# Optimization experiments

Hardware: AMD Instinct MI355X
Metric: run time of the kernel (lower is better)

## Reference

```python
import jax, jax.numpy as jnp
import numpy as np
from jax.scipy.linalg import expm

DIM = 64
TIMESTEPS = 1000
BATCH = 1024


def setup_inputs() -> dict:
    key = jax.random.key(0)
    k1, k2 = jax.random.split(key)
    inputs = jax.random.normal(k1, (BATCH, TIMESTEPS, DIM), dtype=jnp.float32)
    # Kernel: skew-symmetric (oscillatory) + small decay so expm(kernel*t) stays
    # bounded for t up to TIMESTEPS-1 (a random dense kernel would overflow).
    a = jax.random.normal(k2, (DIM, DIM), dtype=jnp.float32)
    kernel = 0.01 * (a - a.T) - 0.002 * jnp.eye(DIM, dtype=jnp.float32)
    return {"inputs": inputs, "kernel": kernel}


def reference(inputs, kernel):
    # matrix_exponentials[t] = expm(kernel * t), t = 0..T-1  -> [T, dim, dim]
    ts = jnp.arange(TIMESTEPS, dtype=kernel.dtype)
    mexp = jax.vmap(expm)(kernel[None, :, :] * ts[:, None, None])
    # trajs = einsum('tij,bj->bti'): propagate initial state inputs[:, 0, :]
    x0 = inputs[:, 0, :]  # [B, dim]
    return jnp.einsum('tij,bj->bti', mexp, x0)  # [B, T, dim]
```

## Files before the change

### kernel.cpp

```cpp
#include <hip/hip_runtime.h>

#define NMAT 1000
#define SA_PAD 68
#define LDM 72

#define SEEDF_OFF 2048000
#define X0B_OFF   8355840

typedef short short8 __attribute__((ext_vector_type(8)));
typedef float floatx4 __attribute__((ext_vector_type(4)));
typedef unsigned short ushortx4 __attribute__((ext_vector_type(4)));

__device__ __forceinline__ unsigned short f2bf(float f) {
    unsigned int u = __float_as_uint(f);
    u += 0x7fffu + ((u >> 16) & 1u);
    return (unsigned short)(u >> 16);
}

__device__ __forceinline__ void mm_core(const float* __restrict__ sA,
                                        const float* __restrict__ sB,
                                        int r0, int c0, float acc[4][4])
{
#pragma unroll
    for (int k = 0; k < 64; k += 4) {
        float4 b0 = *(const float4*)&sB[(k + 0) * SA_PAD + c0];
        float4 b1 = *(const float4*)&sB[(k + 1) * SA_PAD + c0];
        float4 b2 = *(const float4*)&sB[(k + 2) * SA_PAD + c0];
        float4 b3 = *(const float4*)&sB[(k + 3) * SA_PAD + c0];
#pragma unroll
        for (int u = 0; u < 4; ++u) {
            float4 a = *(const float4*)&sA[(r0 + u) * SA_PAD + k];
            acc[u][0] += a.x * b0.x + a.y * b1.x + a.z * b2.x + a.w * b3.x;
            acc[u][1] += a.x * b0.y + a.y * b1.y + a.z * b2.y + a.w * b3.y;
            acc[u][2] += a.x * b0.z + a.y * b1.z + a.z * b2.z + a.w * b3.z;
            acc[u][3] += a.x * b0.w + a.y * b1.w + a.z * b2.w + a.w * b3.w;
        }
    }
}

__device__ __forceinline__ void stageLDS(float* __restrict__ s, const float* __restrict__ g, int tid)
{
#pragma unroll
    for (int q = 0; q < 4; ++q) {
        int i4 = tid + 256 * q;
        int r = i4 >> 4, c4 = (i4 & 15) * 4;
        *(float4*)&s[r * SA_PAD + c4] = *(const float4*)&g[i4 * 4];
    }
}

__global__ __launch_bounds__(256) void k_build(const float* __restrict__ K,
                                               const float* __restrict__ in,
                                               float* __restrict__ ws)
{
    const int tid = threadIdx.x;
    unsigned short* tab16 = (unsigned short*)ws;
    unsigned short* x0b = (unsigned short*)((char*)ws + X0B_OFF);

    if (blockIdx.x != 0) {
        const int rb = (blockIdx.x - 1) * 64;
#pragma unroll
        for (int q = 0; q < 4; ++q) {
            int i4 = tid + 256 * q;
            int b = rb + (i4 >> 4), c4 = (i4 & 15) * 4;
            float4 v = *(const float4*)&in[(size_t)b * 64000 + c4];
            ushortx4 h = { f2bf(v.x), f2bf(v.y), f2bf(v.z), f2bf(v.w) };
            *(ushortx4*)&x0b[(size_t)b * 64 + c4] = h;
        }
        return;
    }

    __shared__ __align__(16) float smem[6 * 64 * SA_PAD];

#pragma unroll
    for (int q = 0; q < 4; ++q) {
        int i4 = tid + 256 * q;
        int r = i4 >> 4, c4 = (i4 & 15) * 4;
        *(float4*)&smem[r * SA_PAD + c4] = *(const float4*)&K[i4 * 4];
        ushortx4 id = {0, 0, 0, 0};
        if (r >= c4 && r < c4 + 4) ((unsigned short*)&id)[r - c4] = 0x3F80;
        *(ushortx4*)&tab16[r * 64 + c4] = id;
    }

    const float c1_ = 1.f, c2_ = 0.5f, c3_ = 1.f / 6.f, c4_ = 1.f / 24.f, c5_ = 1.f / 120.f,
                c6_ = 1.f / 720.f, c7_ = 1.f / 5040.f, c8_ = 1.f / 40320.f, c9_ = 1.f / 362880.f,
                c10_ = 1.f / 3628800.f, c11_ = 1.f / 39916800.f, c12_ = 1.f / 479001600.f;

    const signed char SD[14]  = {1, 2, 3, 5, 4, 5, 0, 1, 2, 3, 4, 5, 0, 1};
    const signed char SAi[14] = {0, 1, 1, 4, 5, 4, 5, 0, 1, 2, 3, 4, 5, 0};
    const signed char SBi[14] = {0, 0, 1, 3, 3, 4, 5, 0, 1, 2, 3, 4, 5, 0};
    const signed char SE[14]  = {-1, -1, -1, 0, 1, -1, -1, -1, -1, -1, -1, -1, -1, -1};
    const short       STt[14] = {-1, -1, -1, -1, 1, 2, 4, 8, 16, 32, 64, 128, 256, 512};

    const int r0 = (tid >> 4) * 4, c0 = (tid & 15) * 4;

#pragma unroll 1
    for (int st = 0; st < 14; ++st) {
        if (st == 3) {
            __syncthreads();
#pragma unroll
            for (int s = 0; s < 16; ++s) {
                int idx = tid + 256 * s;
                int r = idx >> 6, c = idx & 63;
                smem[4 * (64 * SA_PAD) + r * SA_PAD + c] =
                      c12_ * smem[3 * (64 * SA_PAD) + r * SA_PAD + c] + (r == c ? c8_ : 0.f)
                    + c9_  * smem[0 * (64 * SA_PAD) + r * SA_PAD + c]
                    + c10_ * smem[1 * (64 * SA_PAD) + r * SA_PAD + c]
                    + c11_ * smem[2 * (64 * SA_PAD) + r * SA_PAD + c];
            }
        }
        __syncthreads();
        const float* A = smem + (int)SAi[st] * (64 * SA_PAD);
        const float* B = smem + (int)SBi[st] * (64 * SA_PAD);
        float acc[4][4] = {};
        mm_core(A, B, r0, c0, acc);

        float cI = 0.f, cK = 0.f, cT2 = 0.f, cT3 = 0.f;
        const int epi = SE[st];
        if (epi == 0) { cI = c4_; cK = c5_; cT2 = c6_; cT3 = c7_; }
        if (epi == 1) { cI = 1.f; cK = c1_; cT2 = c2_; cT3 = c3_; }

        float* D = smem + (int)SD[st] * (64 * SA_PAD);
        float* sf = (STt[st] >= 0) ? (ws + SEEDF_OFF + (size_t)(st - 4) * 4096) : nullptr;
        unsigned short* tb = (STt[st] >= 0) ? (tab16 + (size_t)STt[st] * 4096) : nullptr;
#pragma unroll
        for (int u = 0; u < 4; ++u) {
            int r = r0 + u;
            float o[4];
#pragma unroll
            for (int v = 0; v < 4; ++v) {
                int c = c0 + v;
                float val = acc[u][v];
                if (epi >= 0) {
                    val += (r == c ? cI : 0.f)
                         + cK  * smem[0 * (64 * SA_PAD) + r * SA_PAD + c]
                         + cT2 * smem[1 * (64 * SA_PAD) + r * SA_PAD + c]
                         + cT3 * smem[2 * (64 * SA_PAD) + r * SA_PAD + c];
                }
                o[v] = val;
            }
            float4 vv = {o[0], o[1], o[2], o[3]};
            *(float4*)&D[r * SA_PAD + c0] = vv;
            if (sf) {
                *(float4*)&sf[r * 64 + c0] = vv;
                ushortx4 h = { f2bf(o[0]), f2bf(o[1]), f2bf(o[2]), f2bf(o[3]) };
                *(ushortx4*)&tb[r * 64 + c0] = h;
            }
        }
    }
}

__global__ __launch_bounds__(256) void k_pows(float* __restrict__ ws)
{
    __shared__ __align__(16) float s0[64 * SA_PAD], s1[64 * SA_PAD], s2[64 * SA_PAD];
    const int t = blockIdx.x;
    if (__popc(t) < 2) return;
    const float* seedF = ws + SEEDF_OFF;
    unsigned short* tab16 = (unsigned short*)ws;
    const int tid = threadIdx.x;
    const int r0 = (tid >> 4) * 4, c0 = (tid & 15) * 4;

    float* P = s0;
    float* Bs = s1;
    float* Cs = s2;

    int hb = 31 - __clz(t);
    stageLDS(P, seedF + (size_t)hb * 4096, tid);
    int rem = t & ~(1 << hb);

    float4 rg[4];
    {
        int b = 31 - __clz(rem);
        rem &= ~(1 << b);
        const float* g = seedF + (size_t)b * 4096;
#pragma unroll
        for (int q = 0; q < 4; ++q) rg[q] = *(const float4*)&g[(tid + 256 * q) * 4];
    }

    while (true) {
        __syncthreads();
#pragma unroll
        for (int q = 0; q < 4; ++q) {
            int i4 = tid + 256 * q;
            int rr = i4 >> 4, c4 = (i4 & 15) * 4;
            *(float4*)&Bs[rr * SA_PAD + c4] = rg[q];
        }
        int nb = -1;
        if (rem) {
            nb = 31 - __clz(rem);
            rem &= ~(1 << nb);
            const float* g = seedF + (size_t)nb * 4096;
#pragma unroll
            for (int q = 0; q < 4; ++q) rg[q] = *(const float4*)&g[(tid + 256 * q) * 4];
        }
        __syncthreads();
        float acc[4][4] = {};
        mm_core(P, Bs, r0, c0, acc);

        if (nb < 0) {
            unsigned short* C = tab16 + (size_t)t * 4096;
#pragma unroll
            for (int u = 0; u < 4; ++u) {
                ushortx4 h = { f2bf(acc[u][0]), f2bf(acc[u][1]),
                               f2bf(acc[u][2]), f2bf(acc[u][3]) };
                *(ushortx4*)&C[(r0 + u) * 64 + c0] = h;
            }
            return;
        }
#pragma unroll
        for (int u = 0; u < 4; ++u) {
            float4 vv = {acc[u][0], acc[u][1], acc[u][2], acc[u][3]};
            *(float4*)&Cs[(r0 + u) * SA_PAD + c0] = vv;
        }
        float* tmp = P; P = Cs; Cs = tmp;
    }
}

__global__ __launch_bounds__(256) void k_out(const float* __restrict__ ws,
                                             float* __restrict__ out)
{
    __shared__ __align__(16) unsigned short lM[64 * LDM];
    __shared__ __align__(16) unsigned short lX[128 * LDM];

    const unsigned short* tab16 = (const unsigned short*)ws;
    const unsigned short* x0b = (const unsigned short*)((const char*)ws + X0B_OFF);

    const int bx = blockIdx.x;
    const int t = bx >> 3;
    const int b0 = (bx & 7) * 128;
    const unsigned short* Mt = tab16 + (size_t)t * 4096;
    const int tid = threadIdx.x;

#pragma unroll
    for (int q = 0; q < 2; ++q) {
        int i8 = tid + 256 * q;
        int i = i8 >> 3, j8 = (i8 & 7) * 8;
        *(short8*)&lM[i * LDM + j8] = *(const short8*)&Mt[i8 * 8];
    }
#pragma unroll
    for (int q = 0; q < 4; ++q) {
        int i8 = tid + 256 * q;
        int bb = i8 >> 3, j8 = (i8 & 7) * 8;
        *(short8*)&lX[bb * LDM + j8] = *(const short8*)&x0b[(size_t)(b0 + bb) * 64 + j8];
    }
    __syncthreads();

    const int lane = tid & 63;
    const int w = tid >> 6;
    const int m = lane & 15;
    const int kg = lane >> 4;

#pragma unroll
    for (int mt = 0; mt < 2; ++mt) {
        const int mtile = w * 2 + mt;
        short8 a0 = *(const short8*)&lX[(mtile * 16 + m) * LDM + kg * 8];
        short8 a1 = *(const short8*)&lX[(mtile * 16 + m) * LDM + 32 + kg * 8];
#pragma unroll
        for (int n = 0; n < 4; ++n) {
            short8 bf0 = *(const short8*)&lM[(n * 16 + m) * LDM + kg * 8];
            short8 bf1 = *(const short8*)&lM[(n * 16 + m) * LDM + 32 + kg * 8];
            floatx4 acc = {0.f, 0.f, 0.f, 0.f};
            acc = __builtin_amdgcn_mfma_f32_16x16x32_bf16(a0, bf0, acc, 0, 0, 0);
            acc = __builtin_amdgcn_mfma_f32_16x16x32_bf16(a1, bf1, acc, 0, 0, 0);
            size_t base = (size_t)(b0 + mtile * 16 + kg * 4) * 64000 + (size_t)t * 64 + n * 16 + m;
            out[base + 0 * 64000] = acc[0];
            out[base + 1 * 64000] = acc[1];
            out[base + 2 * 64000] = acc[2];
            out[base + 3 * 64000] = acc[3];
        }
    }
}

extern "C" void kernel_launch(void* const* d_in, const int* in_sizes, int n_in,
                              void* d_out, int out_size, void* d_ws, size_t ws_size,
                              hipStream_t stream)
{
    const float* inp = (const float*)d_in[0];
    const float* K   = (const float*)d_in[1];
    float* out = (float*)d_out;
    float* ws  = (float*)d_ws;

    hipLaunchKernelGGL(k_build, dim3(17), dim3(256), 0, stream, K, inp, ws);
    hipLaunchKernelGGL(k_pows, dim3(NMAT), dim3(256), 0, stream, ws);
    hipLaunchKernelGGL(k_out, dim3(8000), dim3(256), 0, stream, ws, out);
}
```

Measured before the change: 590.8 us.

## Swap MFMA operands in output kernel for vectorized stores and drop LDS staging

The output kernel now passes the matrix as the A operand and x0 as the B operand, so each lane holds four consecutive output columns and can write one 16-byte vector store instead of four scattered scalar stores. The LDS staging and barrier are gone: operands load straight from global memory into registers, x0 is loaded once per thread, and each block loops over 8 timesteps with a 64-row batch tile. This targets the write-bandwidth-bound output of about 262 MB by coalescing stores along the contiguous dim axis, at the cost of repeated global reads of matrix tiles, which are expected to hit in cache.

```diff
diff --git a/kernel.cpp b/kernel.cpp
--- a/kernel.cpp
+++ b/kernel.cpp
@@ -2,7 +2,6 @@
 
 #define NMAT 1000
 #define SA_PAD 68
-#define LDM 72
 
 #define SEEDF_OFF 2048000
 #define X0B_OFF   8355840
@@ -218,54 +217,41 @@
 __global__ __launch_bounds__(256) void k_out(const float* __restrict__ ws,
                                              float* __restrict__ out)
 {
-    __shared__ __align__(16) unsigned short lM[64 * LDM];
-    __shared__ __align__(16) unsigned short lX[128 * LDM];
-
     const unsigned short* tab16 = (const unsigned short*)ws;
     const unsigned short* x0b = (const unsigned short*)((const char*)ws + X0B_OFF);
 
     const int bx = blockIdx.x;
-    const int t = bx >> 3;
-    const int b0 = (bx & 7) * 128;
-    const unsigned short* Mt = tab16 + (size_t)t * 4096;
+    const int tg = bx >> 4;
+    const int bt = bx & 15;
     const int tid = threadIdx.x;
-
-#pragma unroll
-    for (int q = 0; q < 2; ++q) {
-        int i8 = tid + 256 * q;
-        int i = i8 >> 3, j8 = (i8 & 7) * 8;
-        *(short8*)&lM[i * LDM + j8] = *(const short8*)&Mt[i8 * 8];
-    }
-#pragma unroll
-    for (int q = 0; q < 4; ++q) {
-        int i8 = tid + 256 * q;
-        int bb = i8 >> 3, j8 = (i8 & 7) * 8;
-        *(short8*)&lX[bb * LDM + j8] = *(const short8*)&x0b[(size_t)(b0 + bb) * 64 + j8];
-    }
-    __syncthreads();
-
     const int lane = tid & 63;
     const int w = tid >> 6;
     const int m = lane & 15;
     const int kg = lane >> 4;
 
-#pragma unroll
-    for (int mt = 0; mt < 2; ++mt) {
-        const int mtile = w * 2 + mt;
-        short8 a0 = *(const short8*)&lX[(mtile * 16 + m) * LDM + kg * 8];
-        short8 a1 = *(const short8*)&lX[(mtile * 16 + m) * LDM + 32 + kg * 8];
+    const int b = bt * 64 + w * 16 + m;
+    const int t0 = tg * 8;
+
+    short8 xb0 = *(const short8*)&x0b[(size_t)b * 64 + kg * 8];
+    short8 xb1 = *(const short8*)&x0b[(size_t)b * 64 + 32 + kg * 8];
+
+    float* outb = out + (size_t)b * 64000 + (size_t)t0 * 64;
+
+#pragma unroll 2
+    for (int tt = 0; tt < 8; ++tt) {
+        const unsigned short* Mt = tab16 + (size_t)(t0 + tt) * 4096;
+        short8 ma[4][2];
 #pragma unroll
         for (int n = 0; n < 4; ++n) {
-            short8 bf0 = *(const short8*)&lM[(n * 16 + m) * LDM + kg * 8];
-            short8 bf1 = *(const short8*)&lM[(n * 16 + m) * LDM + 32 + kg * 8];
+            ma[n][0] = *(const short8*)&Mt[(n * 16 + m) * 64 + kg * 8];
+            ma[n][1] = *(const short8*)&Mt[(n * 16 + m) * 64 + 32 + kg * 8];
+        }
+#pragma unroll
+        for (int n = 0; n < 4; ++n) {
             floatx4 acc = {0.f, 0.f, 0.f, 0.f};
-            acc = __builtin_amdgcn_mfma_f32_16x16x32_bf16(a0, bf0, acc, 0, 0, 0);
-            acc = __builtin_amdgcn_mfma_f32_16x16x32_bf16(a1, bf1, acc, 0, 0, 0);
-            size_t base = (size_t)(b0 + mtile * 16 + kg * 4) * 64000 + (size_t)t * 64 + n * 16 + m;
-            out[base + 0 * 64000] = acc[0];
-            out[base + 1 * 64000] = acc[1];
-            out[base + 2 * 64000] = acc[2];
-            out[base + 3 * 64000] = acc[3];
+            acc = __builtin_amdgcn_mfma_f32_16x16x32_bf16(ma[n][0], xb0, acc, 0, 0, 0);
+            acc = __builtin_amdgcn_mfma_f32_16x16x32_bf16(ma[n][1], xb1, acc, 0, 0, 0);
+            *(floatx4*)&outb[(size_t)tt * 64 + n * 16 + kg * 4] = acc;
         }
     }
 }
@@ -281,5 +267,5 @@
 
     hipLaunchKernelGGL(k_build, dim3(17), dim3(256), 0, stream, K, inp, ws);
     hipLaunchKernelGGL(k_pows, dim3(NMAT), dim3(256), 0, stream, ws);
-    hipLaunchKernelGGL(k_out, dim3(8000), dim3(256), 0, stream, ws, out);
-}
+    hipLaunchKernelGGL(k_out, dim3(2000), dim3(256), 0, stream, ws, out);
+}
```

After: 627.6 us. +6.2%, slower.

## Swap MFMA operands for vectorized output stores and batch eight timesteps per block

Applied to the files above, without the earlier changes.

Swaps the A/B operands of the output MFMA so each lane holds four consecutive output columns, which allows 16-byte float4 stores instead of four strided scalar stores per tile. The batch x0 fragments are loaded once into registers, and each block now loops over 8 timesteps, reloading only the matrix tile. The grid shrinks from 8000 to 1000 blocks. This is meant to cut store transaction count and redundant x0 staging, at the cost of fewer blocks and two barriers per timestep.

```diff
diff --git a/kernel.cpp b/kernel.cpp
--- a/kernel.cpp
+++ b/kernel.cpp
@@ -219,54 +219,59 @@
                                              float* __restrict__ out)
 {
     __shared__ __align__(16) unsigned short lM[64 * LDM];
-    __shared__ __align__(16) unsigned short lX[128 * LDM];
 
     const unsigned short* tab16 = (const unsigned short*)ws;
     const unsigned short* x0b = (const unsigned short*)((const char*)ws + X0B_OFF);
 
     const int bx = blockIdx.x;
-    const int t = bx >> 3;
+    const int tg = bx >> 3;
     const int b0 = (bx & 7) * 128;
-    const unsigned short* Mt = tab16 + (size_t)t * 4096;
+    const int t0 = tg * 8;
     const int tid = threadIdx.x;
-
-#pragma unroll
-    for (int q = 0; q < 2; ++q) {
-        int i8 = tid + 256 * q;
-        int i = i8 >> 3, j8 = (i8 & 7) * 8;
-        *(short8*)&lM[i * LDM + j8] = *(const short8*)&Mt[i8 * 8];
-    }
-#pragma unroll
-    for (int q = 0; q < 4; ++q) {
-        int i8 = tid + 256 * q;
-        int bb = i8 >> 3, j8 = (i8 & 7) * 8;
-        *(short8*)&lX[bb * LDM + j8] = *(const short8*)&x0b[(size_t)(b0 + bb) * 64 + j8];
-    }
-    __syncthreads();
-
     const int lane = tid & 63;
     const int w = tid >> 6;
     const int m = lane & 15;
     const int kg = lane >> 4;
 
+    short8 xb[2][2];
 #pragma unroll
     for (int mt = 0; mt < 2; ++mt) {
-        const int mtile = w * 2 + mt;
-        short8 a0 = *(const short8*)&lX[(mtile * 16 + m) * LDM + kg * 8];
-        short8 a1 = *(const short8*)&lX[(mtile * 16 + m) * LDM + 32 + kg * 8];
+        const int b = b0 + (w * 2 + mt) * 16 + m;
+        xb[mt][0] = *(const short8*)&x0b[(size_t)b * 64 + kg * 8];
+        xb[mt][1] = *(const short8*)&x0b[(size_t)b * 64 + 32 + kg * 8];
+    }
+
+#pragma unroll 1
+    for (int tt = 0; tt < 8; ++tt) {
+        const int t = t0 + tt;
+        const unsigned short* Mt = tab16 + (size_t)t * 4096;
+#pragma unroll
+        for (int q = 0; q < 2; ++q) {
+            int i8 = tid + 256 * q;
+            int i = i8 >> 3, j8 = (i8 & 7) * 8;
+            *(short8*)&lM[i * LDM + j8] = *(const short8*)&Mt[i8 * 8];
+        }
+        __syncthreads();
+
+        short8 ma[4][2];
 #pragma unroll
         for (int n = 0; n < 4; ++n) {
-            short8 bf0 = *(const short8*)&lM[(n * 16 + m) * LDM + kg * 8];
-            short8 bf1 = *(const short8*)&lM[(n * 16 + m) * LDM + 32 + kg * 8];
-            floatx4 acc = {0.f, 0.f, 0.f, 0.f};
-            acc = __builtin_amdgcn_mfma_f32_16x16x32_bf16(a0, bf0, acc, 0, 0, 0);
-            acc = __builtin_amdgcn_mfma_f32_16x16x32_bf16(a1, bf1, acc, 0, 0, 0);
-            size_t base = (size_t)(b0 + mtile * 16 + kg * 4) * 64000 + (size_t)t * 64 + n * 16 + m;
-            out[base + 0 * 64000] = acc[0];
-            out[base + 1 * 64000] = acc[1];
-            out[base + 2 * 64000] = acc[2];
-            out[base + 3 * 64000] = acc[3];
-        }
+            ma[n][0] = *(const short8*)&lM[(n * 16 + m) * LDM + kg * 8];
+            ma[n][1] = *(const short8*)&lM[(n * 16 + m) * LDM + 32 + kg * 8];
+        }
+#pragma unroll
+        for (int mt = 0; mt < 2; ++mt) {
+            const int b = b0 + (w * 2 + mt) * 16 + m;
+            float* outb = out + (size_t)b * 64000 + (size_t)t * 64;
+#pragma unroll
+            for (int n = 0; n < 4; ++n) {
+                floatx4 acc = {0.f, 0.f, 0.f, 0.f};
+                acc = __builtin_amdgcn_mfma_f32_16x16x32_bf16(ma[n][0], xb[mt][0], acc, 0, 0, 0);
+                acc = __builtin_amdgcn_mfma_f32_16x16x32_bf16(ma[n][1], xb[mt][1], acc, 0, 0, 0);
+                *(floatx4*)&outb[n * 16 + kg * 4] = acc;
+            }
+        }
+        __syncthreads();
     }
 }
 
@@ -281,5 +286,5 @@
 
     hipLaunchKernelGGL(k_build, dim3(17), dim3(256), 0, stream, K, inp, ws);
     hipLaunchKernelGGL(k_pows, dim3(NMAT), dim3(256), 0, stream, ws);
-    hipLaunchKernelGGL(k_out, dim3(8000), dim3(256), 0, stream, ws, out);
-}
+    hipLaunchKernelGGL(k_out, dim3(1000), dim3(256), 0, stream, ws, out);
+}
```

After: 602.4 us. About the same (+2.0%).
